# Optimization experiments

Measured on AMD Instinct MI355X. Metric: run time of the kernel, lower is better.

The kernel has to match this reference:

```python
import jax, jax.numpy as jnp
import numpy as np

B, S, D = 1, 2048, 2048
H, DH, DHID, DKER = 16, 128, 128, 64
EPS = 1e-6

def _gelu(x):
    return jax.nn.gelu(x, approximate=False)  # torch F.gelu default is exact erf

def setup_inputs() -> dict:
    key = jax.random.key(0)
    ks = jax.random.split(key, 12)
    inp = {
        'q': jax.random.normal(ks[0], (B, S, D), jnp.float32),
        'k': jax.random.normal(ks[1], (B, S, D), jnp.float32),
        'v': jax.random.normal(ks[2], (B, S, D), jnp.float32),
        'lr_attn_mask': jax.random.randint(ks[3], (1, 1, S, S), 0, 2) > 0,
        'sparse_norms_lse': jax.random.normal(ks[4], (B, H, S, 1), jnp.float32),
        'sparse_attn_weights': jax.random.normal(ks[5], (B, H, S, S), jnp.float32) * 0.1,
        'kernel_q_mat1': jax.random.normal(ks[6], (H, DH, DHID), jnp.float32) * 0.05,
        'kernel_k_mat1': jax.random.normal(ks[7], (H, DH, DHID), jnp.float32) * 0.05,
        'kernel_q_mat2': jax.random.normal(ks[8], (H, DHID, DKER), jnp.float32) * 0.05,
        'kernel_k_mat2': jax.random.normal(ks[9], (H, DHID, DKER), jnp.float32) * 0.05,
        'interaction_k': jax.random.normal(ks[10], (H, DKER, DKER), jnp.float32) * 0.05,
        'scalingD': jnp.ones((1, H, 1, DKER), jnp.float32) * 1e-4,
        'scalingD2': jnp.ones((1, H, 1, DKER), jnp.float32) * 1e-4,
    }
    return inp

def reference(q, k, v, lr_attn_mask, sparse_norms_lse, sparse_attn_weights,
              kernel_q_mat1, kernel_k_mat1, kernel_q_mat2, kernel_k_mat2,
              interaction_k, scalingD, scalingD2):
    b, s, d = q.shape
    dh = d // H
    # [B,S,D] -> [B,H,S,dh]
    q = q.reshape(b, s, H, dh).transpose(0, 2, 1, 3)
    k = k.reshape(b, s, H, dh).transpose(0, 2, 1, 3)
    v = v.reshape(b, s, H, dh).transpose(0, 2, 1, 3)
    # per-head kernel feature maps (dropout is identity, p=0.0)
    q = _gelu(jnp.einsum('bhsd,hde->bhse', q, kernel_q_mat1))
    q = _gelu(jnp.einsum('bhsd,hde->bhse', q, kernel_q_mat2))
    k = _gelu(jnp.einsum('bhsd,hde->bhse', k, kernel_k_mat1))
    k = jnp.abs(scalingD) * _gelu(jnp.einsum('bhsd,hde->bhse', k, kernel_k_mat2))
    k = k + jnp.einsum('bhse,hef->bhsf', k, interaction_k) * scalingD2
    # low-rank kernelized scores: [B,H,S,S]
    out = jnp.einsum('bhse,bhte->bhst', jnp.abs(q), jnp.abs(k))
    mask = lr_attn_mask  # bool, broadcasts over [B,H,S,S]
    out = jnp.where(mask, out, 0.0)
    lr_norms_lse = jnp.log(out.sum(axis=-1, keepdims=True) + EPS)
    norm_factor_lse = jnp.logaddexp(lr_norms_lse, sparse_norms_lse)
    # log-domain merge of low-rank and sparse scores
    out = jnp.where(mask, jnp.log(out + EPS), sparse_attn_weights)
    out = jnp.exp(out - norm_factor_lse)
    out = jnp.einsum('bhst,bhtd->bhsd', out, v)
    return out.transpose(0, 2, 1, 3).reshape(b, s, d)
```

## Files before the change

### kernel.cpp

```cpp
#include <hip/hip_runtime.h>
#include <math.h>

#define S 2048
#define DD 2048
#define NH 16
#define DH 128
#define DHID 128
#define DKER 64
#define EPSF 1e-6f

typedef __attribute__((ext_vector_type(8))) short bf16x8;
typedef __attribute__((ext_vector_type(4))) float f32x4;

__device__ __forceinline__ float gelu_f(float x) {
    return 0.5f * x * (1.0f + erff(x * 0.7071067811865475f));
}

__device__ __forceinline__ ushort f2b(float x) {
    uint32_t u = __float_as_uint(x);
    uint32_t r = (u + 0x7FFFu + ((u >> 16) & 1u)) >> 16;
    return (ushort)r;
}

__device__ __forceinline__ bf16x8 pack8(float4 a, float4 b) {
    bf16x8 r;
    r[0] = (short)f2b(a.x); r[1] = (short)f2b(a.y);
    r[2] = (short)f2b(a.z); r[3] = (short)f2b(a.w);
    r[4] = (short)f2b(b.x); r[5] = (short)f2b(b.y);
    r[6] = (short)f2b(b.z); r[7] = (short)f2b(b.w);
    return r;
}

__global__ __launch_bounds__(256) void k_wprep(const float* __restrict__ wq1,
                                               const float* __restrict__ wk1,
                                               const float* __restrict__ wq2,
                                               const float* __restrict__ wk2,
                                               const float* __restrict__ ik,
                                               ushort* __restrict__ w1qt,
                                               ushort* __restrict__ w1kt,
                                               ushort* __restrict__ w2qt,
                                               ushort* __restrict__ w2kt,
                                               ushort* __restrict__ ikt) {
    const int h = blockIdx.x, m = blockIdx.y, tid = threadIdx.x;
    const float* src; ushort* dst; int E, D;
    if (m == 0)      { src = wq1 + h * 16384; dst = w1qt + h * 16384; E = 128; D = 128; }
    else if (m == 1) { src = wk1 + h * 16384; dst = w1kt + h * 16384; E = 128; D = 128; }
    else if (m == 2) { src = wq2 + h * 8192;  dst = w2qt + h * 8192;  E = 64;  D = 128; }
    else if (m == 3) { src = wk2 + h * 8192;  dst = w2kt + h * 8192;  E = 64;  D = 128; }
    else             { src = ik  + h * 4096;  dst = ikt  + h * 4096;  E = 64;  D = 64;  }
    const int dsh = (D == 128) ? 7 : 6;
    const int n = E * D;
    for (int idx = tid; idx < n; idx += 256) {
        int e = idx >> dsh, d = idx & (D - 1);
        dst[idx] = f2b(src[d * E + e]);
    }
}

__global__ __launch_bounds__(256) void k_fq(const float* __restrict__ X,
                                            const ushort* __restrict__ w1t,
                                            const ushort* __restrict__ w2t,
                                            ushort* __restrict__ Q2) {
    const int h = blockIdx.y;
    const int s0 = blockIdx.x * 64;
    const int tid = threadIdx.x;
    const int wv = tid >> 6, lane = tid & 63;
    const int ln = lane & 15, quad = lane >> 4;
    __shared__ ushort Y1s[64][136];

    const float* Xr = X + (size_t)(s0 + wv * 16 + ln) * DD + h * DH;
    bf16x8 a1[4];
    #pragma unroll
    for (int ks = 0; ks < 4; ++ks)
        a1[ks] = pack8(*(const float4*)(Xr + ks * 32 + quad * 8),
                       *(const float4*)(Xr + ks * 32 + quad * 8 + 4));

    const ushort* W1h = w1t + (size_t)h * DH * DHID;
    f32x4 c1[8];
    #pragma unroll
    for (int n = 0; n < 8; ++n) c1[n] = (f32x4){0.f, 0.f, 0.f, 0.f};
    #pragma unroll
    for (int n = 0; n < 8; ++n)
        #pragma unroll
        for (int ks = 0; ks < 4; ++ks) {
            bf16x8 b = *(const bf16x8*)(W1h + (size_t)(n * 16 + ln) * DHID +
                                        ks * 32 + quad * 8);
            c1[n] = __builtin_amdgcn_mfma_f32_16x16x32_bf16(a1[ks], b, c1[n], 0, 0, 0);
        }
    #pragma unroll
    for (int n = 0; n < 8; ++n)
        #pragma unroll
        for (int r = 0; r < 4; ++r)
            Y1s[wv * 16 + quad * 4 + r][n * 16 + ln] = f2b(gelu_f(c1[n][r]));

    bf16x8 a2[4];
    #pragma unroll
    for (int ks = 0; ks < 4; ++ks)
        a2[ks] = *(const bf16x8*)&Y1s[wv * 16 + ln][ks * 32 + quad * 8];
    const ushort* W2h = w2t + (size_t)h * DKER * DHID;
    f32x4 c2[4];
    #pragma unroll
    for (int n = 0; n < 4; ++n) c2[n] = (f32x4){0.f, 0.f, 0.f, 0.f};
    #pragma unroll
    for (int n = 0; n < 4; ++n)
        #pragma unroll
        for (int ks = 0; ks < 4; ++ks) {
            bf16x8 b = *(const bf16x8*)(W2h + (size_t)(n * 16 + ln) * DHID +
                                        ks * 32 + quad * 8);
            c2[n] = __builtin_amdgcn_mfma_f32_16x16x32_bf16(a2[ks], b, c2[n], 0, 0, 0);
        }
    #pragma unroll
    for (int n = 0; n < 4; ++n)
        #pragma unroll
        for (int r = 0; r < 4; ++r)
            Q2[((size_t)h * S + s0 + wv * 16 + quad * 4 + r) * DKER + n * 16 + ln] =
                f2b(fabsf(gelu_f(c2[n][r])));
}

__global__ __launch_bounds__(256) void k_fk(const float* __restrict__ X,
                                            const ushort* __restrict__ w1t,
                                            const ushort* __restrict__ w2t,
                                            const ushort* __restrict__ ikt,
                                            const float* __restrict__ sD,
                                            const float* __restrict__ sD2,
                                            ushort* __restrict__ K3) {
    const int h = blockIdx.y;
    const int s0 = blockIdx.x * 64;
    const int tid = threadIdx.x;
    const int wv = tid >> 6, lane = tid & 63;
    const int ln = lane & 15, quad = lane >> 4;
    __shared__ ushort Y1s[64][136];
    __shared__ ushort K2s[64][72];

    const float* Xr = X + (size_t)(s0 + wv * 16 + ln) * DD + h * DH;
    bf16x8 a1[4];
    #pragma unroll
    for (int ks = 0; ks < 4; ++ks)
        a1[ks] = pack8(*(const float4*)(Xr + ks * 32 + quad * 8),
                       *(const float4*)(Xr + ks * 32 + quad * 8 + 4));

    const ushort* W1h = w1t + (size_t)h * DH * DHID;
    f32x4 c1[8];
    #pragma unroll
    for (int n = 0; n < 8; ++n) c1[n] = (f32x4){0.f, 0.f, 0.f, 0.f};
    #pragma unroll
    for (int n = 0; n < 8; ++n)
        #pragma unroll
        for (int ks = 0; ks < 4; ++ks) {
            bf16x8 b = *(const bf16x8*)(W1h + (size_t)(n * 16 + ln) * DHID +
                                        ks * 32 + quad * 8);
            c1[n] = __builtin_amdgcn_mfma_f32_16x16x32_bf16(a1[ks], b, c1[n], 0, 0, 0);
        }
    #pragma unroll
    for (int n = 0; n < 8; ++n)
        #pragma unroll
        for (int r = 0; r < 4; ++r)
            Y1s[wv * 16 + quad * 4 + r][n * 16 + ln] = f2b(gelu_f(c1[n][r]));

    bf16x8 a2[4];
    #pragma unroll
    for (int ks = 0; ks < 4; ++ks)
        a2[ks] = *(const bf16x8*)&Y1s[wv * 16 + ln][ks * 32 + quad * 8];
    const ushort* W2h = w2t + (size_t)h * DKER * DHID;
    f32x4 c2[4];
    #pragma unroll
    for (int n = 0; n < 4; ++n) c2[n] = (f32x4){0.f, 0.f, 0.f, 0.f};
    #pragma unroll
    for (int n = 0; n < 4; ++n)
        #pragma unroll
        for (int ks = 0; ks < 4; ++ks) {
            bf16x8 b = *(const bf16x8*)(W2h + (size_t)(n * 16 + ln) * DHID +
                                        ks * 32 + quad * 8);
            c2[n] = __builtin_amdgcn_mfma_f32_16x16x32_bf16(a2[ks], b, c2[n], 0, 0, 0);
        }
    float k2v[4][4];
    float sdv[4], sd2v[4];
    #pragma unroll
    for (int n = 0; n < 4; ++n) {
        sdv[n]  = fabsf(sD[h * DKER + n * 16 + ln]);
        sd2v[n] = sD2[h * DKER + n * 16 + ln];
    }
    #pragma unroll
    for (int n = 0; n < 4; ++n)
        #pragma unroll
        for (int r = 0; r < 4; ++r) {
            k2v[n][r] = sdv[n] * gelu_f(c2[n][r]);
            K2s[wv * 16 + quad * 4 + r][n * 16 + ln] = f2b(k2v[n][r]);
        }
    bf16x8 a3[2];
    #pragma unroll
    for (int ks = 0; ks < 2; ++ks)
        a3[ks] = *(const bf16x8*)&K2s[wv * 16 + ln][ks * 32 + quad * 8];
    const ushort* Ikh = ikt + (size_t)h * DKER * DKER;
    f32x4 c3[4];
    #pragma unroll
    for (int n = 0; n < 4; ++n) c3[n] = (f32x4){0.f, 0.f, 0.f, 0.f};
    #pragma unroll
    for (int n = 0; n < 4; ++n)
        #pragma unroll
        for (int ks = 0; ks < 2; ++ks) {
            bf16x8 b = *(const bf16x8*)(Ikh + (size_t)(n * 16 + ln) * DKER +
                                        ks * 32 + quad * 8);
            c3[n] = __builtin_amdgcn_mfma_f32_16x16x32_bf16(a3[ks], b, c3[n], 0, 0, 0);
        }
    #pragma unroll
    for (int n = 0; n < 4; ++n)
        #pragma unroll
        for (int r = 0; r < 4; ++r)
            K3[((size_t)h * S + s0 + wv * 16 + quad * 4 + r) * DKER + n * 16 + ln] =
                f2b(fabsf(k2v[n][r] + c3[n][r] * sd2v[n]));
}

__global__ __launch_bounds__(256) void k_vt(const float* __restrict__ V,
                                            ushort* __restrict__ Vt) {
    const int h = blockIdx.y;
    const int t0 = blockIdx.x * 64;
    const int tid = threadIdx.x;
    __shared__ ushort Ls[128][72];
    #pragma unroll
    for (int it = 0; it < 8; ++it) {
        int idx = it * 256 + tid;
        int r = idx >> 5, c4 = idx & 31;
        float4 v = *(const float4*)(V + (size_t)(t0 + r) * DD + h * DH + c4 * 4);
        Ls[c4 * 4 + 0][r] = f2b(v.x);
        Ls[c4 * 4 + 1][r] = f2b(v.y);
        Ls[c4 * 4 + 2][r] = f2b(v.z);
        Ls[c4 * 4 + 3][r] = f2b(v.w);
    }
    __syncthreads();
    #pragma unroll
    for (int it = 0; it < 4; ++it) {
        int idx = it * 256 + tid;
        int row = idx >> 3, cc = idx & 7;
        *(bf16x8*)(Vt + ((size_t)h * DH + row) * S + t0 + cc * 8) =
            *(const bf16x8*)(&Ls[row][cc * 8]);
    }
}

__global__ __launch_bounds__(256) void k_mpack(const int* __restrict__ mask,
                                               uint* __restrict__ pm) {
    const int gw = blockIdx.x * 4 + (threadIdx.x >> 6);
    const int lane = threadIdx.x & 63;
    const int row = gw >> 5;
    const int w64 = gw & 31;
    int mv = mask[(size_t)row * S + w64 * 64 + lane];
    unsigned long long b = __ballot(mv != 0);
    if (lane == 0)  pm[row * 64 + w64 * 2]     = (uint)b;
    if (lane == 32) pm[row * 64 + w64 * 2 + 1] = (uint)(b >> 32);
}

__global__ __launch_bounds__(256, 4) void k_attn(const ushort* __restrict__ Q2,
                                                 const ushort* __restrict__ K3,
                                                 const ushort* __restrict__ Vt,
                                                 const uint* __restrict__ pm,
                                                 const float* __restrict__ Wsp,
                                                 float* __restrict__ Op,
                                                 float* __restrict__ rsp) {
    const int h = blockIdx.y;
    const int s0 = blockIdx.x * 64;
    const int z = blockIdx.z;
    const int tbase = z * (S / 2);
    const int tid = threadIdx.x;
    const int wv = tid >> 6, lane = tid & 63;
    const int ln = lane & 15, quad = lane >> 4;
    __shared__ ushort K3s[64][72];
    __shared__ ushort Vts[128][72];
    __shared__ ushort Ps[4][16][72];

    const ushort* K3h = K3 + (size_t)h * S * DKER;
    const ushort* Vth = Vt + (size_t)h * DH * S;
    const float*  Wh  = Wsp + (size_t)h * S * S;
    const int srow_q = s0 + wv * 16 + quad * 4;

    bf16x8 aq[2];
    #pragma unroll
    for (int ks = 0; ks < 2; ++ks)
        aq[ks] = *(const bf16x8*)(Q2 + ((size_t)h * S + s0 + wv * 16 + ln) * DKER +
                                  ks * 32 + quad * 8);

    f32x4 O[8];
    #pragma unroll
    for (int v = 0; v < 8; ++v) O[v] = (f32x4){0.f, 0.f, 0.f, 0.f};
    float rs[4] = {0.f, 0.f, 0.f, 0.f};

    for (int it = 0; it < 16; ++it) {
        const int t0 = tbase + it * 64;
        __syncthreads();
        #pragma unroll
        for (int c = 0; c < 2; ++c) {
            int idx = c * 256 + tid;
            int r = idx >> 3, cc = idx & 7;
            *(bf16x8*)&K3s[r][cc * 8] =
                *(const bf16x8*)(K3h + (size_t)(t0 + r) * DKER + cc * 8);
        }
        #pragma unroll
        for (int c = 0; c < 4; ++c) {
            int idx = c * 256 + tid;
            int r = idx >> 3, cc = idx & 7;
            *(bf16x8*)&Vts[r][cc * 8] =
                *(const bf16x8*)(Vth + (size_t)r * S + t0 + cc * 8);
        }
        __syncthreads();
        uint2 mw[4];
        #pragma unroll
        for (int r = 0; r < 4; ++r)
            mw[r] = *(const uint2*)(pm + (size_t)(srow_q + r) * 64 + (t0 >> 5));
        float ww[4][4];
        #pragma unroll
        for (int n = 0; n < 4; ++n)
            #pragma unroll
            for (int r = 0; r < 4; ++r)
                ww[n][r] = Wh[(size_t)(srow_q + r) * S + t0 + n * 16 + ln];

        f32x4 sc[4];
        #pragma unroll
        for (int n = 0; n < 4; ++n) sc[n] = (f32x4){0.f, 0.f, 0.f, 0.f};
        #pragma unroll
        for (int ks = 0; ks < 2; ++ks)
            #pragma unroll
            for (int n = 0; n < 4; ++n) {
                bf16x8 bf = *(const bf16x8*)&K3s[n * 16 + ln][ks * 32 + quad * 8];
                sc[n] = __builtin_amdgcn_mfma_f32_16x16x32_bf16(aq[ks], bf, sc[n], 0, 0, 0);
            }
        #pragma unroll
        for (int n = 0; n < 4; ++n)
            #pragma unroll
            for (int r = 0; r < 4; ++r) {
                uint word = (n >= 2) ? mw[r].y : mw[r].x;
                int m = (word >> (((n & 1) << 4) + ln)) & 1;
                float s = sc[n][r];
                float p;
                if (m) { rs[r] += s; p = s + EPSF; }
                else   { p = __expf(ww[n][r]); }
                Ps[wv][quad * 4 + r][n * 16 + ln] = f2b(p);
            }
        #pragma unroll
        for (int ks = 0; ks < 2; ++ks) {
            bf16x8 pf = *(const bf16x8*)&Ps[wv][ln][ks * 32 + quad * 8];
            #pragma unroll
            for (int v = 0; v < 8; ++v) {
                bf16x8 vf = *(const bf16x8*)&Vts[v * 16 + ln][ks * 32 + quad * 8];
                O[v] = __builtin_amdgcn_mfma_f32_16x16x32_bf16(pf, vf, O[v], 0, 0, 0);
            }
        }
    }
    #pragma unroll
    for (int r = 0; r < 4; ++r) {
        float v = rs[r];
        v += __shfl_xor(v, 1); v += __shfl_xor(v, 2);
        v += __shfl_xor(v, 4); v += __shfl_xor(v, 8);
        rs[r] = v;
    }
    if (ln == 0) {
        #pragma unroll
        for (int r = 0; r < 4; ++r)
            rsp[((size_t)z * NH + h) * S + srow_q + r] = rs[r];
    }
    #pragma unroll
    for (int v = 0; v < 8; ++v)
        #pragma unroll
        for (int r = 0; r < 4; ++r)
            Op[(((size_t)z * NH + h) * S + srow_q + r) * DH + v * 16 + ln] = O[v][r];
}

__global__ __launch_bounds__(256) void k_comb(const float* __restrict__ Op,
                                              const float* __restrict__ rsp,
                                              const float* __restrict__ lse,
                                              float* __restrict__ out) {
    const int h = blockIdx.y;
    const int s0 = blockIdx.x * 64;
    const int tid = threadIdx.x;
    const int c = (tid & 31) * 4;
    const int r0 = tid >> 5;
    for (int rr = r0; rr < 64; rr += 8) {
        const int row = s0 + rr;
        float rs = rsp[(size_t)h * S + row] + rsp[((size_t)NH + h) * S + row];
        float idv = 1.f / (rs + EPSF + expf(lse[(size_t)h * S + row]));
        float4 a = *(const float4*)(Op + ((size_t)h * S + row) * DH + c);
        float4 b = *(const float4*)(Op + (((size_t)NH + h) * S + row) * DH + c);
        float4 o;
        o.x = (a.x + b.x) * idv; o.y = (a.y + b.y) * idv;
        o.z = (a.z + b.z) * idv; o.w = (a.w + b.w) * idv;
        *(float4*)(out + (size_t)row * DD + h * DH + c) = o;
    }
}

extern "C" void kernel_launch(void* const* d_in, const int* in_sizes, int n_in,
                              void* d_out, int out_size, void* d_ws, size_t ws_size,
                              hipStream_t stream) {
    const float* q   = (const float*)d_in[0];
    const float* k   = (const float*)d_in[1];
    const float* v   = (const float*)d_in[2];
    const int*   msk = (const int*)d_in[3];
    const float* lse = (const float*)d_in[4];
    const float* spw = (const float*)d_in[5];
    const float* wq1 = (const float*)d_in[6];
    const float* wk1 = (const float*)d_in[7];
    const float* wq2 = (const float*)d_in[8];
    const float* wk2 = (const float*)d_in[9];
    const float* ik  = (const float*)d_in[10];
    const float* sD  = (const float*)d_in[11];
    const float* sD2 = (const float*)d_in[12];
    float* out = (float*)d_out;

    ushort* q2b  = (ushort*)d_ws;
    ushort* k3b  = q2b + (size_t)NH * S * DKER;
    ushort* vt   = k3b + (size_t)NH * S * DKER;
    uint*   pm   = (uint*)(vt + (size_t)NH * DH * S);
    ushort* w1qt = (ushort*)(pm + (size_t)S * 64);
    ushort* w1kt = w1qt + (size_t)NH * DH * DHID;
    ushort* w2qt = w1kt + (size_t)NH * DH * DHID;
    ushort* w2kt = w2qt + (size_t)NH * DKER * DHID;
    ushort* ikt  = w2kt + (size_t)NH * DKER * DHID;
    float*  Op   = (float*)(ikt + (size_t)NH * DKER * DKER);
    float*  rsp  = Op + (size_t)2 * NH * S * DH;

    dim3 g(S / 64, NH), b(256);
    k_wprep<<<dim3(NH, 5), b, 0, stream>>>(wq1, wk1, wq2, wk2, ik,
                                           w1qt, w1kt, w2qt, w2kt, ikt);
    k_mpack<<<dim3(S * 32 / 4), b, 0, stream>>>(msk, pm);
    k_vt<<<g, b, 0, stream>>>(v, vt);
    k_fq<<<g, b, 0, stream>>>(q, w1qt, w2qt, q2b);
    k_fk<<<g, b, 0, stream>>>(k, w1kt, w2kt, ikt, sD, sD2, k3b);
    k_attn<<<dim3(S / 64, NH, 2), b, 0, stream>>>(q2b, k3b, vt, pm, spw, Op, rsp);
    k_comb<<<g, b, 0, stream>>>(Op, rsp, lse, out);
}
```

Measured before the change: 515.8 us.

## Drop split-K attention, register-prefetch tiles, fuse feature kernels and combine

```diff
diff --git a/kernel.cpp b/kernel.cpp
--- a/kernel.cpp
+++ b/kernel.cpp
@@ -42,12 +42,13 @@
                                                ushort* __restrict__ w2kt,
                                                ushort* __restrict__ ikt) {
     const int h = blockIdx.x, m = blockIdx.y, tid = threadIdx.x;
-    const float* src; ushort* dst; int E, D;
-    if (m == 0)      { src = wq1 + h * 16384; dst = w1qt + h * 16384; E = 128; D = 128; }
-    else if (m == 1) { src = wk1 + h * 16384; dst = w1kt + h * 16384; E = 128; D = 128; }
-    else if (m == 2) { src = wq2 + h * 8192;  dst = w2qt + h * 8192;  E = 64;  D = 128; }
-    else if (m == 3) { src = wk2 + h * 8192;  dst = w2kt + h * 8192;  E = 64;  D = 128; }
-    else             { src = ik  + h * 4096;  dst = ikt  + h * 4096;  E = 64;  D = 64;  }
+    const float* src; ushort* dst; int D;
+    if (m == 0)      { src = wq1 + h * 16384; dst = w1qt + h * 16384; D = 128; }
+    else if (m == 1) { src = wk1 + h * 16384; dst = w1kt + h * 16384; D = 128; }
+    else if (m == 2) { src = wq2 + h * 8192;  dst = w2qt + h * 8192;  D = 128; }
+    else if (m == 3) { src = wk2 + h * 8192;  dst = w2kt + h * 8192;  D = 128; }
+    else             { src = ik  + h * 4096;  dst = ikt  + h * 4096;  D = 64;  }
+    const int E = (m == 0 || m == 1) ? 128 : 64;
     const int dsh = (D == 128) ? 7 : 6;
     const int n = E * D;
     for (int idx = tid; idx < n; idx += 256) {
@@ -56,16 +57,29 @@
     }
 }
 
-__global__ __launch_bounds__(256) void k_fq(const float* __restrict__ X,
-                                            const ushort* __restrict__ w1t,
-                                            const ushort* __restrict__ w2t,
-                                            ushort* __restrict__ Q2) {
+__global__ __launch_bounds__(256) void k_fused(const float* __restrict__ Xq,
+                                               const float* __restrict__ Xk,
+                                               const ushort* __restrict__ w1qt,
+                                               const ushort* __restrict__ w1kt,
+                                               const ushort* __restrict__ w2qt,
+                                               const ushort* __restrict__ w2kt,
+                                               const ushort* __restrict__ ikt,
+                                               const float* __restrict__ sD,
+                                               const float* __restrict__ sD2,
+                                               ushort* __restrict__ Q2,
+                                               ushort* __restrict__ K3) {
     const int h = blockIdx.y;
     const int s0 = blockIdx.x * 64;
+    const int z = blockIdx.z;
     const int tid = threadIdx.x;
     const int wv = tid >> 6, lane = tid & 63;
     const int ln = lane & 15, quad = lane >> 4;
     __shared__ ushort Y1s[64][136];
+    __shared__ ushort K2s[64][72];
+
+    const float* X = z ? Xk : Xq;
+    const ushort* w1t = z ? w1kt : w1qt;
+    const ushort* w2t = z ? w2kt : w2qt;
 
     const float* Xr = X + (size_t)(s0 + wv * 16 + ln) * DD + h * DH;
     bf16x8 a1[4];
@@ -108,70 +122,17 @@
                                         ks * 32 + quad * 8);
             c2[n] = __builtin_amdgcn_mfma_f32_16x16x32_bf16(a2[ks], b, c2[n], 0, 0, 0);
         }
-    #pragma unroll
-    for (int n = 0; n < 4; ++n)
-        #pragma unroll
-        for (int r = 0; r < 4; ++r)
-            Q2[((size_t)h * S + s0 + wv * 16 + quad * 4 + r) * DKER + n * 16 + ln] =
-                f2b(fabsf(gelu_f(c2[n][r])));
-}
-
-__global__ __launch_bounds__(256) void k_fk(const float* __restrict__ X,
-                                            const ushort* __restrict__ w1t,
-                                            const ushort* __restrict__ w2t,
-                                            const ushort* __restrict__ ikt,
-                                            const float* __restrict__ sD,
-                                            const float* __restrict__ sD2,
-                                            ushort* __restrict__ K3) {
-    const int h = blockIdx.y;
-    const int s0 = blockIdx.x * 64;
-    const int tid = threadIdx.x;
-    const int wv = tid >> 6, lane = tid & 63;
-    const int ln = lane & 15, quad = lane >> 4;
-    __shared__ ushort Y1s[64][136];
-    __shared__ ushort K2s[64][72];
-
-    const float* Xr = X + (size_t)(s0 + wv * 16 + ln) * DD + h * DH;
-    bf16x8 a1[4];
-    #pragma unroll
-    for (int ks = 0; ks < 4; ++ks)
-        a1[ks] = pack8(*(const float4*)(Xr + ks * 32 + quad * 8),
-                       *(const float4*)(Xr + ks * 32 + quad * 8 + 4));
-
-    const ushort* W1h = w1t + (size_t)h * DH * DHID;
-    f32x4 c1[8];
-    #pragma unroll
-    for (int n = 0; n < 8; ++n) c1[n] = (f32x4){0.f, 0.f, 0.f, 0.f};
-    #pragma unroll
-    for (int n = 0; n < 8; ++n)
-        #pragma unroll
-        for (int ks = 0; ks < 4; ++ks) {
-            bf16x8 b = *(const bf16x8*)(W1h + (size_t)(n * 16 + ln) * DHID +
-                                        ks * 32 + quad * 8);
-            c1[n] = __builtin_amdgcn_mfma_f32_16x16x32_bf16(a1[ks], b, c1[n], 0, 0, 0);
-        }
-    #pragma unroll
-    for (int n = 0; n < 8; ++n)
-        #pragma unroll
-        for (int r = 0; r < 4; ++r)
-            Y1s[wv * 16 + quad * 4 + r][n * 16 + ln] = f2b(gelu_f(c1[n][r]));
-
-    bf16x8 a2[4];
-    #pragma unroll
-    for (int ks = 0; ks < 4; ++ks)
-        a2[ks] = *(const bf16x8*)&Y1s[wv * 16 + ln][ks * 32 + quad * 8];
-    const ushort* W2h = w2t + (size_t)h * DKER * DHID;
-    f32x4 c2[4];
-    #pragma unroll
-    for (int n = 0; n < 4; ++n) c2[n] = (f32x4){0.f, 0.f, 0.f, 0.f};
-    #pragma unroll
-    for (int n = 0; n < 4; ++n)
-        #pragma unroll
-        for (int ks = 0; ks < 4; ++ks) {
-            bf16x8 b = *(const bf16x8*)(W2h + (size_t)(n * 16 + ln) * DHID +
-                                        ks * 32 + quad * 8);
-            c2[n] = __builtin_amdgcn_mfma_f32_16x16x32_bf16(a2[ks], b, c2[n], 0, 0, 0);
-        }
+
+    if (z == 0) {
+        #pragma unroll
+        for (int n = 0; n < 4; ++n)
+            #pragma unroll
+            for (int r = 0; r < 4; ++r)
+                Q2[((size_t)h * S + s0 + wv * 16 + quad * 4 + r) * DKER + n * 16 + ln] =
+                    f2b(fabsf(gelu_f(c2[n][r])));
+        return;
+    }
+
     float k2v[4][4];
     float sdv[4], sd2v[4];
     #pragma unroll
@@ -248,17 +209,15 @@
     if (lane == 32) pm[row * 64 + w64 * 2 + 1] = (uint)(b >> 32);
 }
 
-__global__ __launch_bounds__(256, 4) void k_attn(const ushort* __restrict__ Q2,
+__global__ __launch_bounds__(256, 2) void k_attn(const ushort* __restrict__ Q2,
                                                  const ushort* __restrict__ K3,
                                                  const ushort* __restrict__ Vt,
                                                  const uint* __restrict__ pm,
                                                  const float* __restrict__ Wsp,
-                                                 float* __restrict__ Op,
-                                                 float* __restrict__ rsp) {
+                                                 const float* __restrict__ lse,
+                                                 float* __restrict__ out) {
     const int h = blockIdx.y;
     const int s0 = blockIdx.x * 64;
-    const int z = blockIdx.z;
-    const int tbase = z * (S / 2);
     const int tid = threadIdx.x;
     const int wv = tid >> 6, lane = tid & 63;
     const int ln = lane & 15, quad = lane >> 4;
@@ -270,6 +229,7 @@
     const ushort* Vth = Vt + (size_t)h * DH * S;
     const float*  Wh  = Wsp + (size_t)h * S * S;
     const int srow_q = s0 + wv * 16 + quad * 4;
+    const int rk = tid >> 3, ck = tid & 7;
 
     bf16x8 aq[2];
     #pragma unroll
@@ -282,67 +242,73 @@
     for (int v = 0; v < 8; ++v) O[v] = (f32x4){0.f, 0.f, 0.f, 0.f};
     float rs[4] = {0.f, 0.f, 0.f, 0.f};
 
-    for (int it = 0; it < 16; ++it) {
-        const int t0 = tbase + it * 64;
-        __syncthreads();
-        #pragma unroll
-        for (int c = 0; c < 2; ++c) {
-            int idx = c * 256 + tid;
-            int r = idx >> 3, cc = idx & 7;
-            *(bf16x8*)&K3s[r][cc * 8] =
-                *(const bf16x8*)(K3h + (size_t)(t0 + r) * DKER + cc * 8);
-        }
-        #pragma unroll
-        for (int c = 0; c < 4; ++c) {
-            int idx = c * 256 + tid;
-            int r = idx >> 3, cc = idx & 7;
-            *(bf16x8*)&Vts[r][cc * 8] =
-                *(const bf16x8*)(Vth + (size_t)r * S + t0 + cc * 8);
-        }
-        __syncthreads();
-        uint2 mw[4];
-        #pragma unroll
-        for (int r = 0; r < 4; ++r)
-            mw[r] = *(const uint2*)(pm + (size_t)(srow_q + r) * 64 + (t0 >> 5));
-        float ww[4][4];
-        #pragma unroll
-        for (int n = 0; n < 4; ++n)
-            #pragma unroll
-            for (int r = 0; r < 4; ++r)
-                ww[n][r] = Wh[(size_t)(srow_q + r) * S + t0 + n * 16 + ln];
-
-        f32x4 sc[4];
-        #pragma unroll
-        for (int n = 0; n < 4; ++n) sc[n] = (f32x4){0.f, 0.f, 0.f, 0.f};
-        #pragma unroll
-        for (int ks = 0; ks < 2; ++ks)
-            #pragma unroll
-            for (int n = 0; n < 4; ++n) {
-                bf16x8 bf = *(const bf16x8*)&K3s[n * 16 + ln][ks * 32 + quad * 8];
-                sc[n] = __builtin_amdgcn_mfma_f32_16x16x32_bf16(aq[ks], bf, sc[n], 0, 0, 0);
-            }
-        #pragma unroll
-        for (int n = 0; n < 4; ++n)
-            #pragma unroll
-            for (int r = 0; r < 4; ++r) {
-                uint word = (n >= 2) ? mw[r].y : mw[r].x;
-                int m = (word >> (((n & 1) << 4) + ln)) & 1;
-                float s = sc[n][r];
-                float p;
-                if (m) { rs[r] += s; p = s + EPSF; }
-                else   { p = __expf(ww[n][r]); }
-                Ps[wv][quad * 4 + r][n * 16 + ln] = f2b(p);
-            }
-        #pragma unroll
-        for (int ks = 0; ks < 2; ++ks) {
-            bf16x8 pf = *(const bf16x8*)&Ps[wv][ln][ks * 32 + quad * 8];
-            #pragma unroll
-            for (int v = 0; v < 8; ++v) {
-                bf16x8 vf = *(const bf16x8*)&Vts[v * 16 + ln][ks * 32 + quad * 8];
-                O[v] = __builtin_amdgcn_mfma_f32_16x16x32_bf16(pf, vf, O[v], 0, 0, 0);
-            }
-        }
-    }
+    bf16x8 sk[2][2], sv[2][4];
+    float  ww[2][4][4];
+    uint2  mw[2][4];
+
+#define PREF(T, P) do {                                                            \
+    if ((T) < 32) {                                                                \
+        const int t0_ = (T) * 64;                                                  \
+        _Pragma("unroll") for (int c_ = 0; c_ < 2; ++c_)                           \
+            sk[P][c_] = *(const bf16x8*)(K3h +                                     \
+                (size_t)(t0_ + rk + c_ * 32) * DKER + ck * 8);                     \
+        _Pragma("unroll") for (int c_ = 0; c_ < 4; ++c_)                           \
+            sv[P][c_] = *(const bf16x8*)(Vth +                                     \
+                (size_t)(rk + c_ * 32) * S + t0_ + ck * 8);                        \
+        _Pragma("unroll") for (int r_ = 0; r_ < 4; ++r_)                           \
+            mw[P][r_] = *(const uint2*)(pm + (size_t)(srow_q + r_) * 64 +          \
+                                        (t0_ >> 5));                               \
+        _Pragma("unroll") for (int n_ = 0; n_ < 4; ++n_)                           \
+        _Pragma("unroll") for (int r_ = 0; r_ < 4; ++r_)                           \
+            ww[P][n_][r_] = Wh[(size_t)(srow_q + r_) * S + t0_ + n_ * 16 + ln];    \
+    }                                                                              \
+} while (0)
+
+#define STEP(T, P, PN) do {                                                        \
+    __syncthreads();                                 \
+    _Pragma("unroll") for (int c_ = 0; c_ < 2; ++c_)                               \
+        *(bf16x8*)&K3s[rk + c_ * 32][ck * 8] = sk[P][c_];                          \
+    _Pragma("unroll") for (int c_ = 0; c_ < 4; ++c_)                               \
+        *(bf16x8*)&Vts[rk + c_ * 32][ck * 8] = sv[P][c_];                          \
+    __syncthreads();                                      \
+    PREF((T) + 1, PN);      \
+    f32x4 sc[4];                                                                   \
+    _Pragma("unroll") for (int n_ = 0; n_ < 4; ++n_)                               \
+        sc[n_] = (f32x4){0.f, 0.f, 0.f, 0.f};                                      \
+    _Pragma("unroll") for (int ks_ = 0; ks_ < 2; ++ks_)                            \
+    _Pragma("unroll") for (int n_ = 0; n_ < 4; ++n_) {                             \
+        bf16x8 bf = *(const bf16x8*)&K3s[n_ * 16 + ln][ks_ * 32 + quad * 8];       \
+        sc[n_] = __builtin_amdgcn_mfma_f32_16x16x32_bf16(aq[ks_], bf, sc[n_],      \
+                                                         0, 0, 0);                  \
+    }                                                                              \
+    _Pragma("unroll") for (int n_ = 0; n_ < 4; ++n_)                               \
+    _Pragma("unroll") for (int r_ = 0; r_ < 4; ++r_) {                             \
+        uint word = (n_ >= 2) ? mw[P][r_].y : mw[P][r_].x;                         \
+        int m_ = (word >> (((n_ & 1) << 4) + ln)) & 1;                             \
+        float s_ = sc[n_][r_];                                                     \
+        float p_;                                                                  \
+        if (m_) { rs[r_] += s_; p_ = s_ + EPSF; }                                  \
+        else    { p_ = __expf(ww[P][n_][r_]); }                                    \
+        Ps[wv][quad * 4 + r_][n_ * 16 + ln] = f2b(p_);                             \
+    }                                                                              \
+    _Pragma("unroll") for (int ks_ = 0; ks_ < 2; ++ks_) {                          \
+        bf16x8 pf = *(const bf16x8*)&Ps[wv][ln][ks_ * 32 + quad * 8];              \
+        _Pragma("unroll") for (int v_ = 0; v_ < 8; ++v_) {                         \
+            bf16x8 vf = *(const bf16x8*)&Vts[v_ * 16 + ln][ks_ * 32 + quad * 8];   \
+            O[v_] = __builtin_amdgcn_mfma_f32_16x16x32_bf16(pf, vf, O[v_],         \
+                                                            0, 0, 0);               \
+        }                                                                          \
+    }                                                                              \
+} while (0)
+
+    PREF(0, 0);
+    for (int it = 0; it < 32; it += 2) {
+        STEP(it, 0, 1);
+        STEP(it + 1, 1, 0);
+    }
+#undef PREF
+#undef STEP
+
     #pragma unroll
     for (int r = 0; r < 4; ++r) {
         float v = rs[r];
@@ -350,38 +316,15 @@
         v += __shfl_xor(v, 4); v += __shfl_xor(v, 8);
         rs[r] = v;
     }
-    if (ln == 0) {
+    float idv[4];
+    #pragma unroll
+    for (int r = 0; r < 4; ++r)
+        idv[r] = 1.f / (rs[r] + EPSF + expf(lse[(size_t)h * S + srow_q + r]));
+    #pragma unroll
+    for (int v = 0; v < 8; ++v)
         #pragma unroll
         for (int r = 0; r < 4; ++r)
-            rsp[((size_t)z * NH + h) * S + srow_q + r] = rs[r];
-    }
-    #pragma unroll
-    for (int v = 0; v < 8; ++v)
-        #pragma unroll
-        for (int r = 0; r < 4; ++r)
-            Op[(((size_t)z * NH + h) * S + srow_q + r) * DH + v * 16 + ln] = O[v][r];
-}
-
-__global__ __launch_bounds__(256) void k_comb(const float* __restrict__ Op,
-                                              const float* __restrict__ rsp,
-                                              const float* __restrict__ lse,
-                                              float* __restrict__ out) {
-    const int h = blockIdx.y;
-    const int s0 = blockIdx.x * 64;
-    const int tid = threadIdx.x;
-    const int c = (tid & 31) * 4;
-    const int r0 = tid >> 5;
-    for (int rr = r0; rr < 64; rr += 8) {
-        const int row = s0 + rr;
-        float rs = rsp[(size_t)h * S + row] + rsp[((size_t)NH + h) * S + row];
-        float idv = 1.f / (rs + EPSF + expf(lse[(size_t)h * S + row]));
-        float4 a = *(const float4*)(Op + ((size_t)h * S + row) * DH + c);
-        float4 b = *(const float4*)(Op + (((size_t)NH + h) * S + row) * DH + c);
-        float4 o;
-        o.x = (a.x + b.x) * idv; o.y = (a.y + b.y) * idv;
-        o.z = (a.z + b.z) * idv; o.w = (a.w + b.w) * idv;
-        *(float4*)(out + (size_t)row * DD + h * DH + c) = o;
-    }
+            out[(size_t)(srow_q + r) * DD + h * DH + v * 16 + ln] = O[v][r] * idv[r];
 }
 
 extern "C" void kernel_launch(void* const* d_in, const int* in_sizes, int n_in,
@@ -411,16 +354,13 @@
     ushort* w2qt = w1kt + (size_t)NH * DH * DHID;
     ushort* w2kt = w2qt + (size_t)NH * DKER * DHID;
     ushort* ikt  = w2kt + (size_t)NH * DKER * DHID;
-    float*  Op   = (float*)(ikt + (size_t)NH * DKER * DKER);
-    float*  rsp  = Op + (size_t)2 * NH * S * DH;
 
     dim3 g(S / 64, NH), b(256);
     k_wprep<<<dim3(NH, 5), b, 0, stream>>>(wq1, wk1, wq2, wk2, ik,
                                            w1qt, w1kt, w2qt, w2kt, ikt);
     k_mpack<<<dim3(S * 32 / 4), b, 0, stream>>>(msk, pm);
     k_vt<<<g, b, 0, stream>>>(v, vt);
-    k_fq<<<g, b, 0, stream>>>(q, w1qt, w2qt, q2b);
-    k_fk<<<g, b, 0, stream>>>(k, w1kt, w2kt, ikt, sD, sD2, k3b);
-    k_attn<<<dim3(S / 64, NH, 2), b, 0, stream>>>(q2b, k3b, vt, pm, spw, Op, rsp);
-    k_comb<<<g, b, 0, stream>>>(Op, rsp, lse, out);
-}
+    k_fused<<<dim3(S / 64, NH, 2), b, 0, stream>>>(q, k, w1qt, w1kt, w2qt, w2kt,
+                                                   ikt, sD, sD2, q2b, k3b);
+    k_attn<<<g, b, 0, stream>>>(q2b, k3b, vt, pm, spw, lse, out);
+}
```

New measurement: 494.1 us. -4.2%, faster.

## Merge q/k feature kernels into one launch and drop LDS staging in attention

Applied to the files above, without the earlier changes.

```diff
diff --git a/kernel.cpp b/kernel.cpp
--- a/kernel.cpp
+++ b/kernel.cpp
@@ -42,12 +42,13 @@
                                                ushort* __restrict__ w2kt,
                                                ushort* __restrict__ ikt) {
     const int h = blockIdx.x, m = blockIdx.y, tid = threadIdx.x;
-    const float* src; ushort* dst; int E, D;
-    if (m == 0)      { src = wq1 + h * 16384; dst = w1qt + h * 16384; E = 128; D = 128; }
-    else if (m == 1) { src = wk1 + h * 16384; dst = w1kt + h * 16384; E = 128; D = 128; }
-    else if (m == 2) { src = wq2 + h * 8192;  dst = w2qt + h * 8192;  E = 64;  D = 128; }
-    else if (m == 3) { src = wk2 + h * 8192;  dst = w2kt + h * 8192;  E = 64;  D = 128; }
-    else             { src = ik  + h * 4096;  dst = ikt  + h * 4096;  E = 64;  D = 64;  }
+    const float* src; ushort* dst; int D;
+    if (m == 0)      { src = wq1 + h * 16384; dst = w1qt + h * 16384; D = 128; }
+    else if (m == 1) { src = wk1 + h * 16384; dst = w1kt + h * 16384; D = 128; }
+    else if (m == 2) { src = wq2 + h * 8192;  dst = w2qt + h * 8192;  D = 128; }
+    else if (m == 3) { src = wk2 + h * 8192;  dst = w2kt + h * 8192;  D = 128; }
+    else             { src = ik  + h * 4096;  dst = ikt  + h * 4096;  D = 64;  }
+    const int E = (m == 0 || m == 1) ? 128 : 64;
     const int dsh = (D == 128) ? 7 : 6;
     const int n = E * D;
     for (int idx = tid; idx < n; idx += 256) {
@@ -56,81 +57,30 @@
     }
 }
 
-__global__ __launch_bounds__(256) void k_fq(const float* __restrict__ X,
-                                            const ushort* __restrict__ w1t,
-                                            const ushort* __restrict__ w2t,
-                                            ushort* __restrict__ Q2) {
+__global__ __launch_bounds__(256) void k_fused(const float* __restrict__ Xq,
+                                               const float* __restrict__ Xk,
+                                               const ushort* __restrict__ w1qt,
+                                               const ushort* __restrict__ w1kt,
+                                               const ushort* __restrict__ w2qt,
+                                               const ushort* __restrict__ w2kt,
+                                               const ushort* __restrict__ ikt,
+                                               const float* __restrict__ sD,
+                                               const float* __restrict__ sD2,
+                                               ushort* __restrict__ Q2,
+                                               ushort* __restrict__ K3) {
     const int h = blockIdx.y;
     const int s0 = blockIdx.x * 64;
-    const int tid = threadIdx.x;
-    const int wv = tid >> 6, lane = tid & 63;
-    const int ln = lane & 15, quad = lane >> 4;
-    __shared__ ushort Y1s[64][136];
-
-    const float* Xr = X + (size_t)(s0 + wv * 16 + ln) * DD + h * DH;
-    bf16x8 a1[4];
-    #pragma unroll
-    for (int ks = 0; ks < 4; ++ks)
-        a1[ks] = pack8(*(const float4*)(Xr + ks * 32 + quad * 8),
-                       *(const float4*)(Xr + ks * 32 + quad * 8 + 4));
-
-    const ushort* W1h = w1t + (size_t)h * DH * DHID;
-    f32x4 c1[8];
-    #pragma unroll
-    for (int n = 0; n < 8; ++n) c1[n] = (f32x4){0.f, 0.f, 0.f, 0.f};
-    #pragma unroll
-    for (int n = 0; n < 8; ++n)
-        #pragma unroll
-        for (int ks = 0; ks < 4; ++ks) {
-            bf16x8 b = *(const bf16x8*)(W1h + (size_t)(n * 16 + ln) * DHID +
-                                        ks * 32 + quad * 8);
-            c1[n] = __builtin_amdgcn_mfma_f32_16x16x32_bf16(a1[ks], b, c1[n], 0, 0, 0);
-        }
-    #pragma unroll
-    for (int n = 0; n < 8; ++n)
-        #pragma unroll
-        for (int r = 0; r < 4; ++r)
-            Y1s[wv * 16 + quad * 4 + r][n * 16 + ln] = f2b(gelu_f(c1[n][r]));
-
-    bf16x8 a2[4];
-    #pragma unroll
-    for (int ks = 0; ks < 4; ++ks)
-        a2[ks] = *(const bf16x8*)&Y1s[wv * 16 + ln][ks * 32 + quad * 8];
-    const ushort* W2h = w2t + (size_t)h * DKER * DHID;
-    f32x4 c2[4];
-    #pragma unroll
-    for (int n = 0; n < 4; ++n) c2[n] = (f32x4){0.f, 0.f, 0.f, 0.f};
-    #pragma unroll
-    for (int n = 0; n < 4; ++n)
-        #pragma unroll
-        for (int ks = 0; ks < 4; ++ks) {
-            bf16x8 b = *(const bf16x8*)(W2h + (size_t)(n * 16 + ln) * DHID +
-                                        ks * 32 + quad * 8);
-            c2[n] = __builtin_amdgcn_mfma_f32_16x16x32_bf16(a2[ks], b, c2[n], 0, 0, 0);
-        }
-    #pragma unroll
-    for (int n = 0; n < 4; ++n)
-        #pragma unroll
-        for (int r = 0; r < 4; ++r)
-            Q2[((size_t)h * S + s0 + wv * 16 + quad * 4 + r) * DKER + n * 16 + ln] =
-                f2b(fabsf(gelu_f(c2[n][r])));
-}
-
-__global__ __launch_bounds__(256) void k_fk(const float* __restrict__ X,
-                                            const ushort* __restrict__ w1t,
-                                            const ushort* __restrict__ w2t,
-                                            const ushort* __restrict__ ikt,
-                                            const float* __restrict__ sD,
-                                            const float* __restrict__ sD2,
-                                            ushort* __restrict__ K3) {
-    const int h = blockIdx.y;
-    const int s0 = blockIdx.x * 64;
+    const int z = blockIdx.z;
     const int tid = threadIdx.x;
     const int wv = tid >> 6, lane = tid & 63;
     const int ln = lane & 15, quad = lane >> 4;
     __shared__ ushort Y1s[64][136];
     __shared__ ushort K2s[64][72];
 
+    const float* X = z ? Xk : Xq;
+    const ushort* w1t = z ? w1kt : w1qt;
+    const ushort* w2t = z ? w2kt : w2qt;
+
     const float* Xr = X + (size_t)(s0 + wv * 16 + ln) * DD + h * DH;
     bf16x8 a1[4];
     #pragma unroll
@@ -172,6 +122,17 @@
                                         ks * 32 + quad * 8);
             c2[n] = __builtin_amdgcn_mfma_f32_16x16x32_bf16(a2[ks], b, c2[n], 0, 0, 0);
         }
+
+    if (z == 0) {
+        #pragma unroll
+        for (int n = 0; n < 4; ++n)
+            #pragma unroll
+            for (int r = 0; r < 4; ++r)
+                Q2[((size_t)h * S + s0 + wv * 16 + quad * 4 + r) * DKER + n * 16 + ln] =
+                    f2b(fabsf(gelu_f(c2[n][r])));
+        return;
+    }
+
     float k2v[4][4];
     float sdv[4], sd2v[4];
     #pragma unroll
@@ -262,8 +223,6 @@
     const int tid = threadIdx.x;
     const int wv = tid >> 6, lane = tid & 63;
     const int ln = lane & 15, quad = lane >> 4;
-    __shared__ ushort K3s[64][72];
-    __shared__ ushort Vts[128][72];
     __shared__ ushort Ps[4][16][72];
 
     const ushort* K3h = K3 + (size_t)h * S * DKER;
@@ -284,22 +243,6 @@
 
     for (int it = 0; it < 16; ++it) {
         const int t0 = tbase + it * 64;
-        __syncthreads();
-        #pragma unroll
-        for (int c = 0; c < 2; ++c) {
-            int idx = c * 256 + tid;
-            int r = idx >> 3, cc = idx & 7;
-            *(bf16x8*)&K3s[r][cc * 8] =
-                *(const bf16x8*)(K3h + (size_t)(t0 + r) * DKER + cc * 8);
-        }
-        #pragma unroll
-        for (int c = 0; c < 4; ++c) {
-            int idx = c * 256 + tid;
-            int r = idx >> 3, cc = idx & 7;
-            *(bf16x8*)&Vts[r][cc * 8] =
-                *(const bf16x8*)(Vth + (size_t)r * S + t0 + cc * 8);
-        }
-        __syncthreads();
         uint2 mw[4];
         #pragma unroll
         for (int r = 0; r < 4; ++r)
@@ -318,7 +261,8 @@
         for (int ks = 0; ks < 2; ++ks)
             #pragma unroll
             for (int n = 0; n < 4; ++n) {
-                bf16x8 bf = *(const bf16x8*)&K3s[n * 16 + ln][ks * 32 + quad * 8];
+                bf16x8 bf = *(const bf16x8*)(K3h + (size_t)(t0 + n * 16 + ln) * DKER +
+                                             ks * 32 + quad * 8);
                 sc[n] = __builtin_amdgcn_mfma_f32_16x16x32_bf16(aq[ks], bf, sc[n], 0, 0, 0);
             }
         #pragma unroll
@@ -338,7 +282,8 @@
             bf16x8 pf = *(const bf16x8*)&Ps[wv][ln][ks * 32 + quad * 8];
             #pragma unroll
             for (int v = 0; v < 8; ++v) {
-                bf16x8 vf = *(const bf16x8*)&Vts[v * 16 + ln][ks * 32 + quad * 8];
+                bf16x8 vf = *(const bf16x8*)(Vth + (size_t)(v * 16 + ln) * S + t0 +
+                                             ks * 32 + quad * 8);
                 O[v] = __builtin_amdgcn_mfma_f32_16x16x32_bf16(pf, vf, O[v], 0, 0, 0);
             }
         }
@@ -419,8 +364,8 @@
                                            w1qt, w1kt, w2qt, w2kt, ikt);
     k_mpack<<<dim3(S * 32 / 4), b, 0, stream>>>(msk, pm);
     k_vt<<<g, b, 0, stream>>>(v, vt);
-    k_fq<<<g, b, 0, stream>>>(q, w1qt, w2qt, q2b);
-    k_fk<<<g, b, 0, stream>>>(k, w1kt, w2kt, ikt, sD, sD2, k3b);
+    k_fused<<<dim3(S / 64, NH, 2), b, 0, stream>>>(q, k, w1qt, w1kt, w2qt, w2kt,
+                                                   ikt, sD, sD2, q2b, k3b);
     k_attn<<<dim3(S / 64, NH, 2), b, 0, stream>>>(q2b, k3b, vt, pm, spw, Op, rsp);
     k_comb<<<g, b, 0, stream>>>(Op, rsp, lse, out);
 }
```

Result: slower. 612.5 us (+18.7%).
